# Kernel optimization log

Hardware: AMD Instinct MI355X
Metric: run time of the kernel (lower is better)

The kernel has to match this reference:

```python
import jax, jax.numpy as jnp
import numpy as np

B, S, D_IN, D_OUT = 4, 2048, 4096, 16384


def setup_inputs() -> dict:
    key = jax.random.key(0)
    k1, k2, k3, k4 = jax.random.split(key, 4)
    x = jax.random.normal(k1, (B, S, D_IN), dtype=jnp.float32)
    # per-channel symmetric int8 weights, [out_features, in_features]
    weight_int8 = jax.random.randint(k2, (D_OUT, D_IN), -128, 128, dtype=jnp.int32).astype(jnp.int8)
    # per-channel weight scales (positive, realistic magnitude)
    weight_scale = jax.random.uniform(k3, (D_OUT,), dtype=jnp.float32) * 0.01 + 1e-4
    # static per-tensor activation scale (calibrated constant)
    act_scale = jnp.float32(0.02)
    bias = jax.random.normal(k4, (D_OUT,), dtype=jnp.float32) * 0.1
    return {"x": x, "weight_int8": weight_int8, "weight_scale": weight_scale,
            "act_scale": act_scale, "bias": bias}


def reference(x, weight_int8, weight_scale, act_scale, bias):
    orig_shape = x.shape
    orig_dtype = x.dtype
    x2d = x.reshape(-1, orig_shape[-1])  # [M, D_in]
    # static per-tensor symmetric activation quantization
    x_int8 = jnp.clip(jnp.round(x2d.astype(jnp.float32) / act_scale), -128, 127).astype(jnp.int8)
    y_int32 = jnp.matmul(x_int8, weight_int8.T, preferred_element_type=jnp.int32)  # [M, D_out]
    output_scale = (act_scale * weight_scale).astype(jnp.float32)  # [D_out]
    y = y_int32.astype(jnp.float32) * output_scale[None, :] + bias.astype(jnp.float32)[None, :]
    return y.reshape(*orig_shape[:-1], y.shape[-1]).astype(orig_dtype)
```

## Files before the change

kernel.cpp:

```cpp
#include <hip/hip_runtime.h>
#include <stdint.h>

#define GAS __attribute__((address_space(1)))
#define LAS __attribute__((address_space(3)))

typedef int v4i __attribute__((ext_vector_type(4)));

constexpr int Mdim = 8192;
constexpr int Ndim = 16384;
constexpr int Kdim = 4096;

__device__ __forceinline__ int pack4i8(int a, int b, int c, int d) {
    return (a & 255) | ((b & 255) << 8) | ((c & 255) << 16) | ((d & 255) << 24);
}

__device__ __forceinline__ int qz(float v, float inv) {
    return (int)fminf(fmaxf(rintf(v * inv), -128.0f), 127.0f);
}

__global__ void k_quant_x(const float* __restrict__ x, const float* __restrict__ asc,
                          int8_t* __restrict__ xq) {
    const int i = blockIdx.x * blockDim.x + threadIdx.x;
    const float inv = 1.0f / *asc;
    const float4* xv = (const float4*)x + (size_t)i * 4;
    float4 f0 = xv[0], f1 = xv[1], f2 = xv[2], f3 = xv[3];
    int4 o;
    o.x = pack4i8(qz(f0.x, inv), qz(f0.y, inv), qz(f0.z, inv), qz(f0.w, inv));
    o.y = pack4i8(qz(f1.x, inv), qz(f1.y, inv), qz(f1.z, inv), qz(f1.w, inv));
    o.z = pack4i8(qz(f2.x, inv), qz(f2.y, inv), qz(f2.z, inv), qz(f2.w, inv));
    o.w = pack4i8(qz(f3.x, inv), qz(f3.y, inv), qz(f3.z, inv), qz(f3.w, inv));
    ((int4*)xq)[i] = o;
}

__global__ void k_conv_w(const int* __restrict__ w, int8_t* __restrict__ wq) {
    const int i = blockIdx.x * blockDim.x + threadIdx.x;
    const int4* wv = (const int4*)w + (size_t)i * 4;
    int4 a = wv[0], b = wv[1], c = wv[2], d = wv[3];
    int4 o;
    o.x = pack4i8(a.x, a.y, a.z, a.w);
    o.y = pack4i8(b.x, b.y, b.z, b.w);
    o.z = pack4i8(c.x, c.y, c.z, c.w);
    o.w = pack4i8(d.x, d.y, d.z, d.w);
    ((int4*)wq)[i] = o;
}

constexpr int KT2 = Kdim / 64;

__global__ __launch_bounds__(512, 2)
void k_gemm256(const int8_t* __restrict__ Aq, const int8_t* __restrict__ Bq,
               const float* __restrict__ wscale, const float* __restrict__ asc,
               const float* __restrict__ bias, float* __restrict__ out) {
    __shared__ __align__(16) int8_t lds[131072];
    const int tid = threadIdx.x, lane = tid & 63, w = tid >> 6;
    const int wm = w >> 2, wn = w & 3;
    const int lrow = lane & 15, kgrp = lane >> 4;

    const int bid = blockIdx.x;
    const int swz = ((bid & 7) << 8) | (bid >> 3);
    const int mt = swz & 31, nt = swz >> 5;
    const int m0 = mt << 8, n0 = nt << 8;

    int8_t* const A_lds = lds;
    int8_t* const B_lds = lds + 65536;

    const int8_t* gA[2];
    const int8_t* gB[2];
#pragma unroll
    for (int j = 0; j < 2; ++j) {
        const int L  = (j << 13) | (w << 10) | (lane << 4);
        const int Ls = L ^ (((lane >> 3) & 3) << 4);
        const int srow = Ls >> 6, skb = Ls & 63;
        gA[j] = Aq + (size_t)(m0 + srow) * Kdim + skb;
        gB[j] = Bq + (size_t)(n0 + srow) * Kdim + skb;
    }

    auto stageA = [&](int tt) {
#pragma unroll
        for (int j = 0; j < 2; ++j) {
            int8_t* d = A_lds + ((tt & 3) << 14) + (j << 13) + (w << 10);
            __builtin_amdgcn_global_load_lds((const GAS void*)(gA[j] + tt * 64),
                                             (LAS void*)d, 16, 0, 0);
        }
    };
    auto stageB = [&](int tt) {
#pragma unroll
        for (int j = 0; j < 2; ++j) {
            int8_t* d = B_lds + ((tt & 3) << 14) + (j << 13) + (w << 10);
            __builtin_amdgcn_global_load_lds((const GAS void*)(gB[j] + tt * 64),
                                             (LAS void*)d, 16, 0, 0);
        }
    };

    const int kc = (kgrp ^ ((lrow >> 1) & 3)) << 4;
    const int arow0 = (wm << 7) + lrow;
    const int brow0 = (wn << 6) + lrow;

    v4i acc[8][4];
#pragma unroll
    for (int i = 0; i < 8; ++i)
#pragma unroll
        for (int j = 0; j < 4; ++j) acc[i][j] = (v4i){0, 0, 0, 0};

    stageA(0); stageB(0); stageA(1); stageB(1);

    v4i bfr[4];

    auto ktile = [&](int t, int vmw, bool iss) {
        const int8_t* As_ = A_lds + ((t & 3) << 14);
        const int8_t* Bs_ = B_lds + ((t & 3) << 14);
        if (iss) stageA(t + 2);
        if (vmw == 6)      asm volatile("s_waitcnt vmcnt(6)" ::: "memory");
        else if (vmw == 4) asm volatile("s_waitcnt vmcnt(4)" ::: "memory");
        else               asm volatile("s_waitcnt vmcnt(0)" ::: "memory");
        __builtin_amdgcn_s_barrier();
        __builtin_amdgcn_sched_barrier(0);
        v4i a[4];
#pragma unroll
        for (int f = 0; f < 4; ++f)
            bfr[f] = *(const v4i*)(Bs_ + (brow0 + f * 16) * 64 + kc);
#pragma unroll
        for (int f = 0; f < 4; ++f)
            a[f] = *(const v4i*)(As_ + (arow0 + f * 16) * 64 + kc);
        __builtin_amdgcn_s_setprio(1);
#pragma unroll
        for (int fi = 0; fi < 4; ++fi)
#pragma unroll
            for (int fj = 0; fj < 4; ++fj)
                acc[fi][fj] = __builtin_amdgcn_mfma_i32_16x16x64_i8(a[fi], bfr[fj], acc[fi][fj], 0, 0, 0);
        __builtin_amdgcn_s_setprio(0);
        if (iss) stageB(t + 2);
        __builtin_amdgcn_s_barrier();
        __builtin_amdgcn_sched_barrier(0);
#pragma unroll
        for (int f = 0; f < 4; ++f)
            a[f] = *(const v4i*)(As_ + (arow0 + 64 + f * 16) * 64 + kc);
        __builtin_amdgcn_s_setprio(1);
#pragma unroll
        for (int fi = 0; fi < 4; ++fi)
#pragma unroll
            for (int fj = 0; fj < 4; ++fj)
                acc[4 + fi][fj] = __builtin_amdgcn_mfma_i32_16x16x64_i8(a[fi], bfr[fj], acc[4 + fi][fj], 0, 0, 0);
        __builtin_amdgcn_s_setprio(0);
    };

    for (int t = 0; t < KT2 - 2; ++t) ktile(t, 6, true);
    ktile(KT2 - 2, 4, false);
    ktile(KT2 - 1, 0, false);

    const float ascale = *asc;
#pragma unroll
    for (int fj = 0; fj < 4; ++fj) {
        const int col = n0 + (wn << 6) + fj * 16 + lrow;
        const float sc = ascale * wscale[col];
        const float bb = bias[col];
#pragma unroll
        for (int mi = 0; mi < 8; ++mi) {
            const int r0 = m0 + (wm << 7) + mi * 16 + (kgrp << 2);
            float* o = out + (size_t)r0 * Ndim + col;
#pragma unroll
            for (int q = 0; q < 4; ++q)
                o[(size_t)q * Ndim] = (float)acc[mi][fj][q] * sc + bb;
        }
    }
}

template <bool AQ, bool BQ>
__global__ __launch_bounds__(256)
void k_gemm(const int8_t* __restrict__ Aq, const float* __restrict__ Xf,
            const int8_t* __restrict__ Bq, const int* __restrict__ W32,
            const float* __restrict__ wscale, const float* __restrict__ asc,
            const float* __restrict__ bias, float* __restrict__ out) {
    constexpr int BM = 128, BN = 128, BK = 64;
    constexpr int KT = Kdim / BK;
    __shared__ __align__(16) int8_t As[2][BM * BK];
    __shared__ __align__(16) int8_t Bs[2][BN * BK];

    const int tid  = threadIdx.x;
    const int lane = tid & 63;
    const int wid  = tid >> 6;
    const int wm = wid >> 1, wn = wid & 1;
    const int lrow = lane & 15, kgrp = lane >> 4;

    const int cpx = gridDim.x >> 3;
    const int swz = ((int)blockIdx.x & 7) * cpx + ((int)blockIdx.x >> 3);
    const int mt = swz & (Mdim / BM - 1);
    const int nt = swz / (Mdim / BM);
    const int m0 = mt * BM, n0 = nt * BN;

    const float ascale = *asc;
    const float inv = 1.0f / ascale;

    v4i acc[4][4];
#pragma unroll
    for (int i = 0; i < 4; ++i)
#pragma unroll
        for (int j = 0; j < 4; ++j) acc[i][j] = (v4i){0, 0, 0, 0};

    auto stage = [&](int buf, int kt) {
        const int k0 = kt * BK;
        if constexpr (AQ) {
            int8_t* ldsp = &As[buf][wid << 10];
            const int8_t* g = Aq + (size_t)(m0 + (tid >> 2)) * Kdim + k0 + ((tid & 3) << 4);
            __builtin_amdgcn_global_load_lds((const GAS void*)g, (LAS void*)ldsp, 16, 0, 0);
            __builtin_amdgcn_global_load_lds((const GAS void*)(g + (size_t)64 * Kdim),
                                             (LAS void*)(ldsp + 4096), 16, 0, 0);
        } else {
            const int row = tid >> 1, cb = (tid & 1) << 5;
            const float4* src = (const float4*)(Xf + (size_t)(m0 + row) * Kdim + k0 + cb);
            int t[8];
#pragma unroll
            for (int j = 0; j < 8; ++j) {
                float4 f = src[j];
                t[j] = pack4i8(qz(f.x, inv), qz(f.y, inv), qz(f.z, inv), qz(f.w, inv));
            }
            int4* dst = (int4*)&As[buf][row * BK + cb];
            dst[0] = make_int4(t[0], t[1], t[2], t[3]);
            dst[1] = make_int4(t[4], t[5], t[6], t[7]);
        }
        if constexpr (BQ) {
            int8_t* ldsp = &Bs[buf][wid << 10];
            const int8_t* g = Bq + (size_t)(n0 + (tid >> 2)) * Kdim + k0 + ((tid & 3) << 4);
            __builtin_amdgcn_global_load_lds((const GAS void*)g, (LAS void*)ldsp, 16, 0, 0);
            __builtin_amdgcn_global_load_lds((const GAS void*)(g + (size_t)64 * Kdim),
                                             (LAS void*)(ldsp + 4096), 16, 0, 0);
        } else {
            const int row = tid >> 1, cb = (tid & 1) << 5;
            const int4* src = (const int4*)(W32 + (size_t)(n0 + row) * Kdim + k0 + cb);
            int t[8];
#pragma unroll
            for (int j = 0; j < 8; ++j) {
                int4 vv = src[j];
                t[j] = pack4i8(vv.x, vv.y, vv.z, vv.w);
            }
            int4* dst = (int4*)&Bs[buf][row * BK + cb];
            dst[0] = make_int4(t[0], t[1], t[2], t[3]);
            dst[1] = make_int4(t[4], t[5], t[6], t[7]);
        }
    };

    stage(0, 0);
    for (int kt = 0; kt < KT; ++kt) {
        const int cur = kt & 1;
        __syncthreads();
        if (kt + 1 < KT) stage(cur ^ 1, kt + 1);

        v4i a[4], b[4];
        const int koff = kgrp << 4;
#pragma unroll
        for (int i = 0; i < 4; ++i) {
            a[i] = *(const v4i*)&As[cur][(wm * 64 + i * 16 + lrow) * BK + koff];
            b[i] = *(const v4i*)&Bs[cur][(wn * 64 + i * 16 + lrow) * BK + koff];
        }
#pragma unroll
        for (int i = 0; i < 4; ++i)
#pragma unroll
            for (int j = 0; j < 4; ++j)
                acc[i][j] = __builtin_amdgcn_mfma_i32_16x16x64_i8(a[i], b[j], acc[i][j], 0, 0, 0);
    }

#pragma unroll
    for (int j = 0; j < 4; ++j) {
        const int col = n0 + wn * 64 + j * 16 + lrow;
        const float sc = ascale * wscale[col];
        const float bb = bias[col];
#pragma unroll
        for (int i = 0; i < 4; ++i) {
            const int r0 = m0 + wm * 64 + i * 16 + (kgrp << 2);
            float* o = out + (size_t)r0 * Ndim + col;
#pragma unroll
            for (int r = 0; r < 4; ++r)
                o[(size_t)r * Ndim] = (float)acc[i][j][r] * sc + bb;
        }
    }
}

extern "C" void kernel_launch(void* const* d_in, const int* in_sizes, int n_in,
                              void* d_out, int out_size, void* d_ws, size_t ws_size,
                              hipStream_t stream) {
    const float* x      = (const float*)d_in[0];
    const int*   w32    = (const int*)d_in[1];
    const float* wscale = (const float*)d_in[2];
    const float* asc    = (const float*)d_in[3];
    const float* bias   = (const float*)d_in[4];
    float* out = (float*)d_out;

    const size_t nx = (size_t)Mdim * Kdim;
    const size_t nw = (size_t)Ndim * Kdim;
    int8_t* xq = (int8_t*)d_ws;
    int8_t* wq = xq + nx;

    const bool haveX = ws_size >= nx;
    const bool haveW = ws_size >= nx + nw;

    if (haveX) k_quant_x<<<(int)(nx / 16 / 256), 256, 0, stream>>>(x, asc, xq);
    if (haveW) k_conv_w<<<(int)(nw / 16 / 256), 256, 0, stream>>>(w32, wq);

    if (haveW) {
        dim3 grid((Mdim / 256) * (Ndim / 256));
        k_gemm256<<<grid, 512, 0, stream>>>(xq, wq, wscale, asc, bias, out);
    } else if (haveX) {
        dim3 grid((Mdim / 128) * (Ndim / 128));
        k_gemm<true, false><<<grid, 256, 0, stream>>>(xq, x, wq, w32, wscale, asc, bias, out);
    } else {
        dim3 grid((Mdim / 128) * (Ndim / 128));
        k_gemm<false, false><<<grid, 256, 0, stream>>>(xq, x, wq, w32, wscale, asc, bias, out);
    }
}
```

Before: 882.5 us.

## Restructure int8 GEMM main loop schedule with per-half barriers and simpler staging

Replaces the unrolled ktile lambda with a rolled K loop. In that loop LDS fragment reads are issued before the global-to-LDS prefetch for tile s+2, with explicit lgkmcnt waits and four barriers per step. Staging addresses are simplified to one row per 4 lanes with XOR column swizzle, and LDS read offsets are precomputed. The aim is better overlap of LDS reads, global prefetch and MFMA, plus fewer address computations. In exchange it adds extra barriers, and the vmcnt waits are placed differently, which could stall the pipeline.

```diff
diff --git a/kernel.cpp b/kernel.cpp
--- a/kernel.cpp
+++ b/kernel.cpp
@@ -44,7 +44,7 @@
     ((int4*)wq)[i] = o;
 }
 
-constexpr int KT2 = Kdim / 64;
+constexpr int NSTEP = Kdim / 64;
 
 __global__ __launch_bounds__(512, 2)
 void k_gemm256(const int8_t* __restrict__ Aq, const int8_t* __restrict__ Bq,
@@ -63,37 +63,28 @@
     int8_t* const A_lds = lds;
     int8_t* const B_lds = lds + 65536;
 
-    const int8_t* gA[2];
-    const int8_t* gB[2];
-#pragma unroll
-    for (int j = 0; j < 2; ++j) {
-        const int L  = (j << 13) | (w << 10) | (lane << 4);
-        const int Ls = L ^ (((lane >> 3) & 3) << 4);
-        const int srow = Ls >> 6, skb = Ls & 63;
-        gA[j] = Aq + (size_t)(m0 + srow) * Kdim + skb;
-        gB[j] = Bq + (size_t)(n0 + srow) * Kdim + skb;
-    }
-
-    auto stageA = [&](int tt) {
-#pragma unroll
-        for (int j = 0; j < 2; ++j) {
-            int8_t* d = A_lds + ((tt & 3) << 14) + (j << 13) + (w << 10);
-            __builtin_amdgcn_global_load_lds((const GAS void*)(gA[j] + tt * 64),
-                                             (LAS void*)d, 16, 0, 0);
-        }
+    const int srow = (w << 4) + (lane >> 2);
+    const int scol = (((lane & 3) ^ ((lane >> 3) & 3)) << 4);
+    const int8_t* gAu0 = Aq + (size_t)(m0 + srow) * Kdim + scol;
+    const int8_t* gAu1 = Aq + (size_t)(m0 + 128 + srow) * Kdim + scol;
+    const int8_t* gBu0 = Bq + (size_t)(n0 + srow) * Kdim + scol;
+    const int8_t* gBu1 = Bq + (size_t)(n0 + 128 + srow) * Kdim + scol;
+    const int dstoff = w << 10;
+
+    auto stageB2 = [&](int s2) {
+        int8_t* base = B_lds + ((s2 & 3) << 14) + dstoff;
+        __builtin_amdgcn_global_load_lds((const GAS void*)(gBu0 + s2 * 64), (LAS void*)base, 16, 0, 0);
+        __builtin_amdgcn_global_load_lds((const GAS void*)(gBu1 + s2 * 64), (LAS void*)(base + 8192), 16, 0, 0);
     };
-    auto stageB = [&](int tt) {
-#pragma unroll
-        for (int j = 0; j < 2; ++j) {
-            int8_t* d = B_lds + ((tt & 3) << 14) + (j << 13) + (w << 10);
-            __builtin_amdgcn_global_load_lds((const GAS void*)(gB[j] + tt * 64),
-                                             (LAS void*)d, 16, 0, 0);
-        }
+    auto stageA2 = [&](int s2) {
+        int8_t* base = A_lds + ((s2 & 3) << 14) + dstoff;
+        __builtin_amdgcn_global_load_lds((const GAS void*)(gAu0 + s2 * 64), (LAS void*)base, 16, 0, 0);
+        __builtin_amdgcn_global_load_lds((const GAS void*)(gAu1 + s2 * 64), (LAS void*)(base + 8192), 16, 0, 0);
     };
 
     const int kc = (kgrp ^ ((lrow >> 1) & 3)) << 4;
-    const int arow0 = (wm << 7) + lrow;
-    const int brow0 = (wn << 6) + lrow;
+    const int arowb = (((wm << 7) + lrow) << 6) + kc;
+    const int browb = (((wn << 6) + lrow) << 6) + kc;
 
     v4i acc[8][4];
 #pragma unroll
@@ -101,51 +92,51 @@
 #pragma unroll
         for (int j = 0; j < 4; ++j) acc[i][j] = (v4i){0, 0, 0, 0};
 
-    stageA(0); stageB(0); stageA(1); stageB(1);
-
-    v4i bfr[4];
-
-    auto ktile = [&](int t, int vmw, bool iss) {
-        const int8_t* As_ = A_lds + ((t & 3) << 14);
-        const int8_t* Bs_ = B_lds + ((t & 3) << 14);
-        if (iss) stageA(t + 2);
-        if (vmw == 6)      asm volatile("s_waitcnt vmcnt(6)" ::: "memory");
-        else if (vmw == 4) asm volatile("s_waitcnt vmcnt(4)" ::: "memory");
-        else               asm volatile("s_waitcnt vmcnt(0)" ::: "memory");
-        __builtin_amdgcn_s_barrier();
+    stageB2(0); stageA2(0); stageB2(1); stageA2(1);
+    asm volatile("s_waitcnt vmcnt(4)" ::: "memory");
+    __builtin_amdgcn_s_barrier();
+
+    v4i a[4], b[4];
+    for (int s = 0; s < NSTEP; ++s) {
+        const int8_t* As_ = A_lds + ((s & 3) << 14);
+        const int8_t* Bs_ = B_lds + ((s & 3) << 14);
+        const bool st = s < NSTEP - 2;
+#pragma unroll
+        for (int f = 0; f < 4; ++f)
+            b[f] = *(const v4i*)(Bs_ + browb + f * 1024);
+#pragma unroll
+        for (int f = 0; f < 4; ++f)
+            a[f] = *(const v4i*)(As_ + arowb + f * 1024);
+        if (st) stageB2(s + 2);
+        __builtin_amdgcn_s_barrier();
+        asm volatile("s_waitcnt lgkmcnt(0)" ::: "memory");
         __builtin_amdgcn_sched_barrier(0);
-        v4i a[4];
+        __builtin_amdgcn_s_setprio(1);
+#pragma unroll
+        for (int fi = 0; fi < 4; ++fi)
+#pragma unroll
+            for (int fj = 0; fj < 4; ++fj)
+                acc[fi][fj] = __builtin_amdgcn_mfma_i32_16x16x64_i8(a[fi], b[fj], acc[fi][fj], 0, 0, 0);
+        __builtin_amdgcn_s_setprio(0);
+        __builtin_amdgcn_s_barrier();
 #pragma unroll
         for (int f = 0; f < 4; ++f)
-            bfr[f] = *(const v4i*)(Bs_ + (brow0 + f * 16) * 64 + kc);
-#pragma unroll
-        for (int f = 0; f < 4; ++f)
-            a[f] = *(const v4i*)(As_ + (arow0 + f * 16) * 64 + kc);
+            a[f] = *(const v4i*)(As_ + arowb + 4096 + f * 1024);
+        if (st) stageA2(s + 2);
+        if (st)                    asm volatile("s_waitcnt vmcnt(4)" ::: "memory");
+        else if (s == NSTEP - 2)   asm volatile("s_waitcnt vmcnt(0)" ::: "memory");
+        __builtin_amdgcn_s_barrier();
+        asm volatile("s_waitcnt lgkmcnt(0)" ::: "memory");
+        __builtin_amdgcn_sched_barrier(0);
         __builtin_amdgcn_s_setprio(1);
 #pragma unroll
         for (int fi = 0; fi < 4; ++fi)
 #pragma unroll
             for (int fj = 0; fj < 4; ++fj)
-                acc[fi][fj] = __builtin_amdgcn_mfma_i32_16x16x64_i8(a[fi], bfr[fj], acc[fi][fj], 0, 0, 0);
+                acc[4 + fi][fj] = __builtin_amdgcn_mfma_i32_16x16x64_i8(a[fi], b[fj], acc[4 + fi][fj], 0, 0, 0);
         __builtin_amdgcn_s_setprio(0);
-        if (iss) stageB(t + 2);
-        __builtin_amdgcn_s_barrier();
-        __builtin_amdgcn_sched_barrier(0);
-#pragma unroll
-        for (int f = 0; f < 4; ++f)
-            a[f] = *(const v4i*)(As_ + (arow0 + 64 + f * 16) * 64 + kc);
-        __builtin_amdgcn_s_setprio(1);
-#pragma unroll
-        for (int fi = 0; fi < 4; ++fi)
-#pragma unroll
-            for (int fj = 0; fj < 4; ++fj)
-                acc[4 + fi][fj] = __builtin_amdgcn_mfma_i32_16x16x64_i8(a[fi], bfr[fj], acc[4 + fi][fj], 0, 0, 0);
-        __builtin_amdgcn_s_setprio(0);
-    };
-
-    for (int t = 0; t < KT2 - 2; ++t) ktile(t, 6, true);
-    ktile(KT2 - 2, 4, false);
-    ktile(KT2 - 1, 0, false);
+        __builtin_amdgcn_s_barrier();
+    }
 
     const float ascale = *asc;
 #pragma unroll
```

After: 823.9 us. 6.6% less time.
